# Optimization experiments

Measured on AMD Instinct MI355X. Metric: run time of the kernel, lower is better.

The kernel has to match this reference:

```python
import jax, jax.numpy as jnp
import numpy as np

TOP_K = 2  # n_heads / k in SigmaMoE


def setup_inputs() -> dict:
    key = jax.random.key(0)
    k1, k2, k3, k4 = jax.random.split(key, 4)
    B, S, d = 4, 2048, 512
    E, H = 32, 128  # n_experts, expert_size
    # init scales mirror reset_parameters (std ~ 1/sqrt(fan_in)) so sigmoid router is unsaturated
    x = jax.random.normal(k1, (B, S, d), dtype=jnp.float32)
    expert_sel = jax.random.normal(k2, (E, d), dtype=jnp.float32) / np.sqrt(d).astype(np.float32)
    keys = jax.random.normal(k3, (E, d, H), dtype=jnp.float32) / np.sqrt(d).astype(np.float32)
    values = jax.random.normal(k4, (E, H, d), dtype=jnp.float32) / np.sqrt(E * H).astype(np.float32)
    return {"x": x, "expert_sel": expert_sel, "keys": keys, "values": values}


def reference(x, expert_sel, keys, values):
    # x: [B, S, d]; expert_sel: [E, d]; keys: [E, d, H]; values: [E, H, v]
    B, S, d = x.shape
    E = keys.shape[0]
    xt = x.reshape(-1, d)                       # [T, d] tokens
    T = xt.shape[0]

    # Router: sigmoid gate + top-k expert selection (eval mode: no dropout, no sel_hist)
    sel = jax.nn.sigmoid(xt @ expert_sel.T)     # [T, E]
    sel_val, sel_idx = jax.lax.top_k(sel, TOP_K)  # [T, K] each; combine is order-invariant

    # Sparse routing weights as dense [T, E] mask (zero for unselected experts,
    # so unselected expert compute is exactly cancelled -> same math as cvmm dispatch/combine)
    w = jnp.zeros((T, E), dtype=xt.dtype).at[jnp.arange(T)[:, None], sel_idx].add(sel_val)

    # Expert FFN: scores = relu(x @ keys[e]); out = sum_e w[t,e] * scores @ values[e]
    h = jax.nn.relu(jnp.einsum('td,edh->teh', xt, keys))   # [T, E, H]
    out = jnp.einsum('teh,te,ehv->tv', h, w, values)       # [T, v]
    return out.reshape(B, S, -1)
```

## Files before the change

### kernel.cpp

```cpp
#include <hip/hip_runtime.h>

#define TT 8192
#define DD 512
#define EE 32
#define HH 128
#define NRB 256

typedef float f32x4 __attribute__((ext_vector_type(4)));
typedef __bf16 bf16x8 __attribute__((ext_vector_type(8)));
typedef unsigned short u16x8 __attribute__((ext_vector_type(8)));

__device__ __forceinline__ unsigned short f2bf(float f) {
  unsigned int u = __builtin_bit_cast(unsigned int, f);
  u = (u + 0x7FFFu + ((u >> 16) & 1u)) >> 16;
  return (unsigned short)u;
}
__device__ __forceinline__ float bf2f(unsigned short h) {
  return __builtin_bit_cast(float, (unsigned int)h << 16);
}

#define GLD16(g, l)                                                            \
  __builtin_amdgcn_global_load_lds(                                            \
      (const __attribute__((address_space(1))) unsigned int*)(g),              \
      (__attribute__((address_space(3))) unsigned int*)(l), 16, 0, 0)

__global__ __launch_bounds__(256) void prep_kernel(
    const float* __restrict__ x, const float* __restrict__ esel,
    const float* __restrict__ keys, const float* __restrict__ values,
    unsigned short* __restrict__ keysT, unsigned short* __restrict__ valuesT,
    unsigned short* __restrict__ xb, int* __restrict__ ccnt,
    int* __restrict__ etok, float* __restrict__ ew) {
  const int tid = threadIdx.x;
  int bid = blockIdx.x;
  if (bid < NRB) {
    __shared__ float ls[2][32][33];
    __shared__ int bcnt[EE], bcur[EE];
    const int tok0 = bid * 32;
    const int wv = tid >> 6, lane = tid & 63;
    const int mh = wv & 1;
    const int kh2 = wv >> 1;
    const int ll = lane & 15, lh = lane >> 4;
    const int row = tok0 + mh * 16 + ll;

    const float* xr = x + (size_t)row * DD + lh * 8;
    unsigned short* xbr = xb + (size_t)row * DD + lh * 8;
    const float* e0 = esel + (size_t)ll * DD + lh * 8;
    const float* e1 = esel + (size_t)(ll + 16) * DD + lh * 8;

    f32x4 acc0, acc1;
    acc0[0] = 0.f; acc0[1] = 0.f; acc0[2] = 0.f; acc0[3] = 0.f;
    acc1 = acc0;

#pragma unroll 2
    for (int kl = 0; kl < 8; kl++) {
      int k = kh2 * 8 + kl;
      float4 v0 = *(const float4*)(xr + k * 32);
      float4 v1 = *(const float4*)(xr + k * 32 + 4);
      float vv[8] = {v0.x, v0.y, v0.z, v0.w, v1.x, v1.y, v1.z, v1.w};
      bf16x8 ah, al, al2;
      unsigned short hs[8];
#pragma unroll
      for (int j = 0; j < 8; j++) {
        unsigned short hh = f2bf(vv[j]);
        float r1 = vv[j] - bf2f(hh);
        unsigned short lo = f2bf(r1);
        float r2 = r1 - bf2f(lo);
        hs[j] = hh;
        ah[j] = __builtin_bit_cast(__bf16, hh);
        al[j] = __builtin_bit_cast(__bf16, lo);
        al2[j] = __builtin_bit_cast(__bf16, f2bf(r2));
      }
      *(ushort4*)(xbr + k * 32) = *(ushort4*)&hs[0];
      *(ushort4*)(xbr + k * 32 + 4) = *(ushort4*)&hs[4];

      float4 c00 = *(const float4*)(e0 + k * 32);
      float4 c01 = *(const float4*)(e0 + k * 32 + 4);
      float4 c10 = *(const float4*)(e1 + k * 32);
      float4 c11 = *(const float4*)(e1 + k * 32 + 4);
      float ea[8] = {c00.x, c00.y, c00.z, c00.w, c01.x, c01.y, c01.z, c01.w};
      float eb[8] = {c10.x, c10.y, c10.z, c10.w, c11.x, c11.y, c11.z, c11.w};
      bf16x8 bh0, bl0, bm0, bh1, bl1, bm1;
#pragma unroll
      for (int j = 0; j < 8; j++) {
        unsigned short hh = f2bf(ea[j]);
        float r1 = ea[j] - bf2f(hh);
        unsigned short lo = f2bf(r1);
        float r2 = r1 - bf2f(lo);
        bh0[j] = __builtin_bit_cast(__bf16, hh);
        bl0[j] = __builtin_bit_cast(__bf16, lo);
        bm0[j] = __builtin_bit_cast(__bf16, f2bf(r2));
        hh = f2bf(eb[j]);
        r1 = eb[j] - bf2f(hh);
        lo = f2bf(r1);
        r2 = r1 - bf2f(lo);
        bh1[j] = __builtin_bit_cast(__bf16, hh);
        bl1[j] = __builtin_bit_cast(__bf16, lo);
        bm1[j] = __builtin_bit_cast(__bf16, f2bf(r2));
      }

      acc0 = __builtin_amdgcn_mfma_f32_16x16x32_bf16(ah, bh0, acc0, 0, 0, 0);
      acc0 = __builtin_amdgcn_mfma_f32_16x16x32_bf16(ah, bl0, acc0, 0, 0, 0);
      acc0 = __builtin_amdgcn_mfma_f32_16x16x32_bf16(al, bh0, acc0, 0, 0, 0);
      acc0 = __builtin_amdgcn_mfma_f32_16x16x32_bf16(ah, bm0, acc0, 0, 0, 0);
      acc0 = __builtin_amdgcn_mfma_f32_16x16x32_bf16(al, bl0, acc0, 0, 0, 0);
      acc0 = __builtin_amdgcn_mfma_f32_16x16x32_bf16(al2, bh0, acc0, 0, 0, 0);

      acc1 = __builtin_amdgcn_mfma_f32_16x16x32_bf16(ah, bh1, acc1, 0, 0, 0);
      acc1 = __builtin_amdgcn_mfma_f32_16x16x32_bf16(ah, bl1, acc1, 0, 0, 0);
      acc1 = __builtin_amdgcn_mfma_f32_16x16x32_bf16(al, bh1, acc1, 0, 0, 0);
      acc1 = __builtin_amdgcn_mfma_f32_16x16x32_bf16(ah, bm1, acc1, 0, 0, 0);
      acc1 = __builtin_amdgcn_mfma_f32_16x16x32_bf16(al, bl1, acc1, 0, 0, 0);
      acc1 = __builtin_amdgcn_mfma_f32_16x16x32_bf16(al2, bh1, acc1, 0, 0, 0);
    }

#pragma unroll
    for (int r = 0; r < 4; r++) {
      ls[kh2][mh * 16 + lh * 4 + r][ll] = acc0[r];
      ls[kh2][mh * 16 + lh * 4 + r][16 + ll] = acc1[r];
    }
    if (tid < EE) bcnt[tid] = 0;
    __syncthreads();

    int i0 = 0, i1 = 0;
    float w0 = 0.f, w1 = 0.f;
    if (tid < 32) {
      float m0 = -3.4e38f;
#pragma unroll
      for (int e2 = 0; e2 < EE; e2++) {
        float v = ls[0][tid][e2] + ls[1][tid][e2];
        if (v > m0) { m0 = v; i0 = e2; }
      }
      float m1 = -3.4e38f;
      i1 = (i0 == 0) ? 1 : 0;
#pragma unroll
      for (int e2 = 0; e2 < EE; e2++) {
        float v = ls[0][tid][e2] + ls[1][tid][e2];
        if (e2 != i0 && v > m1) { m1 = v; i1 = e2; }
      }
      w0 = 1.f / (1.f + expf(-m0));
      w1 = 1.f / (1.f + expf(-m1));
      atomicAdd(&bcnt[i0], 1);
      atomicAdd(&bcnt[i1], 1);
    }
    __syncthreads();
    if (tid < EE) { ccnt[tid * NRB + bid] = bcnt[tid]; bcur[tid] = 0; }
    __syncthreads();
    if (tid < 32) {
      int t = tok0 + tid;
      int p0 = atomicAdd(&bcur[i0], 1);
      etok[((size_t)i0 * NRB + bid) * 32 + p0] = t;
      ew[((size_t)i0 * NRB + bid) * 32 + p0] = w0;
      int p1 = atomicAdd(&bcur[i1], 1);
      etok[((size_t)i1 * NRB + bid) * 32 + p1] = t | (1 << 20);
      ew[((size_t)i1 * NRB + bid) * 32 + p1] = w1;
    }
    return;
  }
  bid -= NRB;
  __shared__ float tile[64][68];
  const float* src;
  unsigned short* dst;
  int R, C, r0, c0, e;
  if (bid < 512) {
    e = bid >> 4; int sub = bid & 15;
    R = DD; C = HH; r0 = (sub >> 1) * 64; c0 = (sub & 1) * 64;
    src = keys; dst = keysT;
  } else {
    bid -= 512;
    e = bid >> 4; int sub = bid & 15;
    R = HH; C = DD; r0 = (sub & 1) * 64; c0 = (sub >> 1) * 64;
    src = values; dst = valuesT;
  }
  const int rl = tid >> 2, cq = (tid & 3) * 16;
  const float* s0 = src + ((size_t)e * R + r0 + rl) * C + c0 + cq;
#pragma unroll
  for (int i = 0; i < 4; i++) *(float4*)&tile[rl][cq + 4 * i] = *(const float4*)(s0 + 4 * i);
  __syncthreads();
  unsigned short* d0 = dst + ((size_t)e * C + c0 + rl) * R + r0 + cq;
#pragma unroll
  for (int i = 0; i < 4; i++) {
    ushort4 v;
    v.x = f2bf(tile[cq + 4 * i + 0][rl]);
    v.y = f2bf(tile[cq + 4 * i + 1][rl]);
    v.z = f2bf(tile[cq + 4 * i + 2][rl]);
    v.w = f2bf(tile[cq + 4 * i + 3][rl]);
    *(ushort4*)(d0 + 4 * i) = v;
  }
}

__global__ __launch_bounds__(512) void moe_gemm_kernel(
    const unsigned short* __restrict__ xb,
    const unsigned short* __restrict__ keysT,
    const unsigned short* __restrict__ valuesT,
    const int* __restrict__ ccnt,
    const int* __restrict__ etok,
    const float* __restrict__ ew,
    unsigned short* __restrict__ yb) {
  const int e = blockIdx.x;
  const int base = blockIdx.y * 64;

  __shared__ int csc[NRB];
  __shared__ unsigned short stage_buf[2][8192];
  __shared__ unsigned short h_swz[8192];
  __shared__ int tok_s[64];
  __shared__ int srow_s[64];
  __shared__ float w_s[64];

  const int tid = threadIdx.x;

  if (tid < NRB) csc[tid] = ccnt[e * NRB + tid];
  __syncthreads();
  for (int off = 1; off < NRB; off <<= 1) {
    int v = 0;
    if (tid < NRB) { v = csc[tid]; if (tid >= off) v += csc[tid - off]; }
    __syncthreads();
    if (tid < NRB) csc[tid] = v;
    __syncthreads();
  }
  const int cnt = csc[NRB - 1];
  if (base >= cnt) return;

  const int lane = tid & 63;
  const int wv = tid >> 6;
  const int wm = wv & 3;
  const int wn = wv >> 2;
  const int ll = lane & 15, lh = lane >> 4;

  const unsigned short* kT = keysT + (size_t)e * HH * DD;
  const unsigned short* vT = valuesT + (size_t)e * DD * HH;

  auto stage_b1 = [&](int c, int b) {
#pragma unroll
    for (int i = 0; i < 2; i++) {
      int P = (i * 512 + tid) * 16;
      int n = P >> 7;
      int q = P & 127;
      const char* g = (const char*)(kT + (size_t)n * DD + c * 64) + (q ^ ((n & 7) << 4));
      char* l = (char*)stage_buf[b] + (i * 512 + (tid & ~63)) * 16;
      GLD16(g, l);
    }
  };
  auto stage_b2 = [&](int c, int b) {
#pragma unroll
    for (int i = 0; i < 2; i++) {
      int P = (i * 512 + tid) * 16;
      int r = P >> 8;
      int q = P & 255;
      const char* g = (const char*)(vT + (size_t)(c * 64 + r) * HH) + (q ^ ((r & 7) << 4));
      char* l = (char*)stage_buf[b] + (i * 512 + (tid & ~63)) * 16;
      GLD16(g, l);
    }
  };

  stage_b1(0, 0);
  if (tid < 64) {
    int i = base + tid;
    bool valid = i < cnt;
    int ie = valid ? i : (cnt - 1);
    int lo = 0, hi = NRB - 1;
    while (lo < hi) { int mid = (lo + hi) >> 1; if (csc[mid] > ie) hi = mid; else lo = mid + 1; }
    int prev = lo ? csc[lo - 1] : 0;
    size_t cell = ((size_t)e * NRB + lo) * 32 + (ie - prev);
    int v = etok[cell];
    int t = v & 0xFFFFF;
    tok_s[tid] = t;
    srow_s[tid] = valid ? ((v >> 20) * (TT + 1) + t) : TT;
    w_s[tid] = valid ? ew[cell] : 0.f;
  }
  __syncthreads();

  const unsigned short* ap = xb + (size_t)tok_s[wm * 16 + ll] * DD;

  f32x4 acc[4];
#pragma unroll
  for (int n = 0; n < 4; n++) { acc[n][0] = 0.f; acc[n][1] = 0.f; acc[n][2] = 0.f; acc[n][3] = 0.f; }

  for (int c = 0; c < 8; c++) {
    if (c < 7) stage_b1(c + 1, (c + 1) & 1);
    else       stage_b2(0, 0);
    const char* sb = (const char*)stage_buf[c & 1];
#pragma unroll
    for (int kkl = 0; kkl < 2; kkl++) {
      bf16x8 af = *(const bf16x8*)(ap + c * 64 + kkl * 32 + lh * 8);
#pragma unroll
      for (int nt = 0; nt < 4; nt++) {
        int n = wn * 64 + nt * 16 + ll;
        int boff = n * 128 + ((kkl * 64 + lh * 16) ^ ((n & 7) << 4));
        bf16x8 bfr = *(const bf16x8*)(sb + boff);
        acc[nt] = __builtin_amdgcn_mfma_f32_16x16x32_bf16(af, bfr, acc[nt], 0, 0, 0);
      }
    }
    __syncthreads();
  }

#pragma unroll
  for (int nt = 0; nt < 4; nt++) {
#pragma unroll
    for (int r = 0; r < 4; r++) {
      int row = wm * 16 + lh * 4 + r;
      int col = wn * 64 + nt * 16 + ll;
      int off = row * 256 + ((col * 2) ^ ((row & 7) << 4));
      *(unsigned short*)((char*)h_swz + off) = f2bf(fmaxf(acc[nt][r], 0.f));
    }
  }
  __syncthreads();

  bf16x8 a2[4];
#pragma unroll
  for (int kk = 0; kk < 4; kk++) {
    int row = wm * 16 + ll;
    int off = row * 256 + ((kk * 64 + lh * 16) ^ ((row & 7) << 4));
    a2[kk] = *(const bf16x8*)((const char*)h_swz + off);
  }

  float wr[4];
#pragma unroll
  for (int r = 0; r < 4; r++) wr[r] = w_s[wm * 16 + lh * 4 + r];

  __syncthreads();
  unsigned short* y_lds = h_swz;

  for (int c = 0; c < 8; c++) {
    if (c < 7) stage_b2(c + 1, (c + 1) & 1);
    const char* sb = (const char*)stage_buf[c & 1];
#pragma unroll
    for (int ntl = 0; ntl < 2; ntl++) {
      f32x4 c2;
      c2[0] = 0.f; c2[1] = 0.f; c2[2] = 0.f; c2[3] = 0.f;
#pragma unroll
      for (int kk = 0; kk < 4; kk++) {
        int r = wn * 32 + ntl * 16 + ll;
        int boff = r * 256 + ((kk * 64 + lh * 16) ^ ((r & 7) << 4));
        bf16x8 bfr = *(const bf16x8*)(sb + boff);
        c2 = __builtin_amdgcn_mfma_f32_16x16x32_bf16(a2[kk], bfr, c2, 0, 0, 0);
      }
      int colb = wn * 32 + ntl * 16 + ll;
#pragma unroll
      for (int r = 0; r < 4; r++) {
        int row = wm * 16 + lh * 4 + r;
        int off = row * 128 + ((colb * 2) ^ ((row & 7) << 4));
        *(unsigned short*)((char*)y_lds + off) = f2bf(c2[r] * wr[r]);
      }
    }
    __syncthreads();
    {
      int rr = tid >> 3, g = tid & 7;
      int off = rr * 128 + ((g * 16) ^ ((rr & 7) << 4));
      u16x8 v = *(const u16x8*)((const char*)y_lds + off);
      *(u16x8*)(yb + (size_t)srow_s[rr] * DD + c * 64 + g * 8) = v;
    }
    __syncthreads();
  }
}

__global__ __launch_bounds__(256) void combine_kernel(const unsigned short* __restrict__ yb,
                                                      float* __restrict__ out) {
  size_t i = ((size_t)blockIdx.x * 256 + threadIdx.x) * 8;
  u16x8 a = *(const u16x8*)(yb + i);
  u16x8 b = *(const u16x8*)(yb + (size_t)(TT + 1) * DD + i);
  float4 o0, o1;
  o0.x = bf2f(a[0]) + bf2f(b[0]);
  o0.y = bf2f(a[1]) + bf2f(b[1]);
  o0.z = bf2f(a[2]) + bf2f(b[2]);
  o0.w = bf2f(a[3]) + bf2f(b[3]);
  o1.x = bf2f(a[4]) + bf2f(b[4]);
  o1.y = bf2f(a[5]) + bf2f(b[5]);
  o1.z = bf2f(a[6]) + bf2f(b[6]);
  o1.w = bf2f(a[7]) + bf2f(b[7]);
  *(float4*)(out + i) = o0;
  *(float4*)(out + i + 4) = o1;
}

extern "C" void kernel_launch(void* const* d_in, const int* in_sizes, int n_in,
                              void* d_out, int out_size, void* d_ws, size_t ws_size,
                              hipStream_t stream) {
  const float* x = (const float*)d_in[0];
  const float* esel = (const float*)d_in[1];
  const float* keys = (const float*)d_in[2];
  const float* values = (const float*)d_in[3];
  float* out = (float*)d_out;

  char* p = (char*)d_ws;
  unsigned short* xb = (unsigned short*)p;      p += (size_t)TT * DD * 2;
  unsigned short* keysT = (unsigned short*)p;   p += (size_t)EE * DD * HH * 2;
  unsigned short* valuesT = (unsigned short*)p; p += (size_t)EE * DD * HH * 2;
  int* ccnt = (int*)p;                          p += (size_t)EE * NRB * 4;
  int* etok = (int*)p;                          p += (size_t)EE * NRB * 32 * 4;
  float* ew = (float*)p;                        p += (size_t)EE * NRB * 32 * 4;
  unsigned short* yb = (unsigned short*)p;      p += (size_t)2 * (TT + 1) * DD * 2;

  prep_kernel<<<NRB + 1024, 256, 0, stream>>>(x, esel, keys, values, keysT, valuesT,
                                              xb, ccnt, etok, ew);
  moe_gemm_kernel<<<dim3(EE, TT / 64), 512, 0, stream>>>(xb, keysT, valuesT, ccnt, etok, ew, yb);
  combine_kernel<<<(TT * DD / 8) / 256, 256, 0, stream>>>(yb, out);
}
```

Before: 51.22 us.

## Precompute per-expert scans and compact work list to replace oversized GEMM grid

```diff
diff --git a/kernel.cpp b/kernel.cpp
--- a/kernel.cpp
+++ b/kernel.cpp
@@ -29,9 +29,10 @@
     const float* __restrict__ keys, const float* __restrict__ values,
     unsigned short* __restrict__ keysT, unsigned short* __restrict__ valuesT,
     unsigned short* __restrict__ xb, int* __restrict__ ccnt,
-    int* __restrict__ etok, float* __restrict__ ew) {
+    int* __restrict__ etok, float* __restrict__ ew, int* __restrict__ wl_cnt) {
   const int tid = threadIdx.x;
   int bid = blockIdx.x;
+  if (bid == 0 && tid == 0) *wl_cnt = 0;
   if (bid < NRB) {
     __shared__ float ls[2][32][33];
     __shared__ int bcnt[EE], bcur[EE];
@@ -188,18 +189,56 @@
   }
 }
 
+__global__ __launch_bounds__(NRB) void scan_kernel(
+    const int* __restrict__ ccnt, const int* __restrict__ etok,
+    const float* __restrict__ ew, int* __restrict__ cntg,
+    int* __restrict__ etok2, float* __restrict__ ew2,
+    int* __restrict__ wl, int* __restrict__ wl_cnt) {
+  __shared__ int csc[NRB];
+  __shared__ int sbase;
+  const int e = blockIdx.x, tid = threadIdx.x;
+  csc[tid] = ccnt[e * NRB + tid];
+  __syncthreads();
+  for (int off = 1; off < NRB; off <<= 1) {
+    int v = csc[tid];
+    if (tid >= off) v += csc[tid - off];
+    __syncthreads();
+    csc[tid] = v;
+    __syncthreads();
+  }
+  const int cnt = csc[NRB - 1];
+  const int s = tid ? csc[tid - 1] : 0;
+  const int c = csc[tid] - s;
+  const int* st = etok + ((size_t)e * NRB + tid) * 32;
+  const float* sw = ew + ((size_t)e * NRB + tid) * 32;
+  for (int j = 0; j < c; j++) {
+    etok2[(size_t)e * TT + s + j] = st[j];
+    ew2[(size_t)e * TT + s + j] = sw[j];
+  }
+  if (tid == 0) {
+    cntg[e] = cnt;
+    sbase = atomicAdd(wl_cnt, (cnt + 63) >> 6);
+  }
+  __syncthreads();
+  if (tid < ((cnt + 63) >> 6)) wl[sbase + tid] = (e << 16) | tid;
+}
+
 __global__ __launch_bounds__(512) void moe_gemm_kernel(
     const unsigned short* __restrict__ xb,
     const unsigned short* __restrict__ keysT,
     const unsigned short* __restrict__ valuesT,
-    const int* __restrict__ ccnt,
-    const int* __restrict__ etok,
-    const float* __restrict__ ew,
+    const int* __restrict__ cntg,
+    const int* __restrict__ etok2,
+    const float* __restrict__ ew2,
+    const int* __restrict__ wl, const int* __restrict__ wl_cnt,
     unsigned short* __restrict__ yb) {
-  const int e = blockIdx.x;
-  const int base = blockIdx.y * 64;
-
-  __shared__ int csc[NRB];
+  const int bid = blockIdx.x;
+  if (bid >= *wl_cnt) return;
+  const int wle = wl[bid];
+  const int e = wle >> 16;
+  const int base = (wle & 0xFFFF) * 64;
+  const int cnt = cntg[e];
+
   __shared__ unsigned short stage_buf[2][8192];
   __shared__ unsigned short h_swz[8192];
   __shared__ int tok_s[64];
@@ -207,19 +246,6 @@
   __shared__ float w_s[64];
 
   const int tid = threadIdx.x;
-
-  if (tid < NRB) csc[tid] = ccnt[e * NRB + tid];
-  __syncthreads();
-  for (int off = 1; off < NRB; off <<= 1) {
-    int v = 0;
-    if (tid < NRB) { v = csc[tid]; if (tid >= off) v += csc[tid - off]; }
-    __syncthreads();
-    if (tid < NRB) csc[tid] = v;
-    __syncthreads();
-  }
-  const int cnt = csc[NRB - 1];
-  if (base >= cnt) return;
-
   const int lane = tid & 63;
   const int wv = tid >> 6;
   const int wm = wv & 3;
@@ -257,15 +283,11 @@
     int i = base + tid;
     bool valid = i < cnt;
     int ie = valid ? i : (cnt - 1);
-    int lo = 0, hi = NRB - 1;
-    while (lo < hi) { int mid = (lo + hi) >> 1; if (csc[mid] > ie) hi = mid; else lo = mid + 1; }
-    int prev = lo ? csc[lo - 1] : 0;
-    size_t cell = ((size_t)e * NRB + lo) * 32 + (ie - prev);
-    int v = etok[cell];
+    int v = etok2[(size_t)e * TT + ie];
     int t = v & 0xFFFFF;
     tok_s[tid] = t;
     srow_s[tid] = valid ? ((v >> 20) * (TT + 1) + t) : TT;
-    w_s[tid] = valid ? ew[cell] : 0.f;
+    w_s[tid] = valid ? ew2[(size_t)e * TT + ie] : 0.f;
   }
   __syncthreads();
 
@@ -387,10 +409,16 @@
   int* ccnt = (int*)p;                          p += (size_t)EE * NRB * 4;
   int* etok = (int*)p;                          p += (size_t)EE * NRB * 32 * 4;
   float* ew = (float*)p;                        p += (size_t)EE * NRB * 32 * 4;
+  int* cntg = (int*)p;                          p += 256;
+  int* etok2 = (int*)p;                         p += (size_t)EE * TT * 4;
+  float* ew2 = (float*)p;                       p += (size_t)EE * TT * 4;
+  int* wl = (int*)p;                            p += 512 * 4;
+  int* wl_cnt = (int*)p;                        p += 256;
   unsigned short* yb = (unsigned short*)p;      p += (size_t)2 * (TT + 1) * DD * 2;
 
   prep_kernel<<<NRB + 1024, 256, 0, stream>>>(x, esel, keys, values, keysT, valuesT,
-                                              xb, ccnt, etok, ew);
-  moe_gemm_kernel<<<dim3(EE, TT / 64), 512, 0, stream>>>(xb, keysT, valuesT, ccnt, etok, ew, yb);
+                                              xb, ccnt, etok, ew, wl_cnt);
+  scan_kernel<<<EE, NRB, 0, stream>>>(ccnt, etok, ew, cntg, etok2, ew2, wl, wl_cnt);
+  moe_gemm_kernel<<<512, 512, 0, stream>>>(xb, keysT, valuesT, cntg, etok2, ew2, wl, wl_cnt, yb);
   combine_kernel<<<(TT * DD / 8) / 256, 256, 0, stream>>>(yb, out);
 }
```

Measured after the change: 54.83 us. 1.07x slower.

## Widen prep kernel to 512 threads and use wave-shuffle prefix scan in GEMM

Applied to the files above, without the earlier changes.

```diff
diff --git a/kernel.cpp b/kernel.cpp
--- a/kernel.cpp
+++ b/kernel.cpp
@@ -24,7 +24,7 @@
       (const __attribute__((address_space(1))) unsigned int*)(g),              \
       (__attribute__((address_space(3))) unsigned int*)(l), 16, 0, 0)
 
-__global__ __launch_bounds__(256) void prep_kernel(
+__global__ __launch_bounds__(512) void prep_kernel(
     const float* __restrict__ x, const float* __restrict__ esel,
     const float* __restrict__ keys, const float* __restrict__ values,
     unsigned short* __restrict__ keysT, unsigned short* __restrict__ valuesT,
@@ -33,12 +33,12 @@
   const int tid = threadIdx.x;
   int bid = blockIdx.x;
   if (bid < NRB) {
-    __shared__ float ls[2][32][33];
+    __shared__ float ls[4][32][33];
     __shared__ int bcnt[EE], bcur[EE];
     const int tok0 = bid * 32;
     const int wv = tid >> 6, lane = tid & 63;
     const int mh = wv & 1;
-    const int kh2 = wv >> 1;
+    const int kq = wv >> 1;
     const int ll = lane & 15, lh = lane >> 4;
     const int row = tok0 + mh * 16 + ll;
 
@@ -52,8 +52,8 @@
     acc1 = acc0;
 
 #pragma unroll 2
-    for (int kl = 0; kl < 8; kl++) {
-      int k = kh2 * 8 + kl;
+    for (int kl = 0; kl < 4; kl++) {
+      int k = kq * 4 + kl;
       float4 v0 = *(const float4*)(xr + k * 32);
       float4 v1 = *(const float4*)(xr + k * 32 + 4);
       float vv[8] = {v0.x, v0.y, v0.z, v0.w, v1.x, v1.y, v1.z, v1.w};
@@ -115,8 +115,8 @@
 
 #pragma unroll
     for (int r = 0; r < 4; r++) {
-      ls[kh2][mh * 16 + lh * 4 + r][ll] = acc0[r];
-      ls[kh2][mh * 16 + lh * 4 + r][16 + ll] = acc1[r];
+      ls[kq][mh * 16 + lh * 4 + r][ll] = acc0[r];
+      ls[kq][mh * 16 + lh * 4 + r][16 + ll] = acc1[r];
     }
     if (tid < EE) bcnt[tid] = 0;
     __syncthreads();
@@ -127,14 +127,14 @@
       float m0 = -3.4e38f;
 #pragma unroll
       for (int e2 = 0; e2 < EE; e2++) {
-        float v = ls[0][tid][e2] + ls[1][tid][e2];
+        float v = ls[0][tid][e2] + ls[1][tid][e2] + ls[2][tid][e2] + ls[3][tid][e2];
         if (v > m0) { m0 = v; i0 = e2; }
       }
       float m1 = -3.4e38f;
       i1 = (i0 == 0) ? 1 : 0;
 #pragma unroll
       for (int e2 = 0; e2 < EE; e2++) {
-        float v = ls[0][tid][e2] + ls[1][tid][e2];
+        float v = ls[0][tid][e2] + ls[1][tid][e2] + ls[2][tid][e2] + ls[3][tid][e2];
         if (e2 != i0 && v > m1) { m1 = v; i1 = e2; }
       }
       w0 = 1.f / (1.f + expf(-m0));
@@ -171,14 +171,14 @@
     R = HH; C = DD; r0 = (sub & 1) * 64; c0 = (sub >> 1) * 64;
     src = values; dst = valuesT;
   }
-  const int rl = tid >> 2, cq = (tid & 3) * 16;
+  const int rl = tid >> 3, cq = (tid & 7) * 8;
   const float* s0 = src + ((size_t)e * R + r0 + rl) * C + c0 + cq;
-#pragma unroll
-  for (int i = 0; i < 4; i++) *(float4*)&tile[rl][cq + 4 * i] = *(const float4*)(s0 + 4 * i);
+  *(float4*)&tile[rl][cq] = *(const float4*)(s0);
+  *(float4*)&tile[rl][cq + 4] = *(const float4*)(s0 + 4);
   __syncthreads();
   unsigned short* d0 = dst + ((size_t)e * C + c0 + rl) * R + r0 + cq;
 #pragma unroll
-  for (int i = 0; i < 4; i++) {
+  for (int i = 0; i < 2; i++) {
     ushort4 v;
     v.x = f2bf(tile[cq + 4 * i + 0][rl]);
     v.y = f2bf(tile[cq + 4 * i + 1][rl]);
@@ -200,6 +200,7 @@
   const int base = blockIdx.y * 64;
 
   __shared__ int csc[NRB];
+  __shared__ int cnt_s;
   __shared__ unsigned short stage_buf[2][8192];
   __shared__ unsigned short h_swz[8192];
   __shared__ int tok_s[64];
@@ -207,21 +208,28 @@
   __shared__ float w_s[64];
 
   const int tid = threadIdx.x;
-
-  if (tid < NRB) csc[tid] = ccnt[e * NRB + tid];
-  __syncthreads();
-  for (int off = 1; off < NRB; off <<= 1) {
-    int v = 0;
-    if (tid < NRB) { v = csc[tid]; if (tid >= off) v += csc[tid - off]; }
-    __syncthreads();
-    if (tid < NRB) csc[tid] = v;
-    __syncthreads();
-  }
-  const int cnt = csc[NRB - 1];
-  if (base >= cnt) return;
-
   const int lane = tid & 63;
   const int wv = tid >> 6;
+
+  if (wv == 0) {
+    int4 c4 = *(const int4*)(ccnt + e * NRB + lane * 4);
+    int s0 = c4.x, s1 = s0 + c4.y, s2 = s1 + c4.z, s3 = s2 + c4.w;
+    int tot = s3;
+    for (int off = 1; off < 64; off <<= 1) {
+      int n = __shfl_up(tot, off);
+      if (lane >= off) tot += n;
+    }
+    int b0 = tot - s3;
+    csc[lane * 4 + 0] = b0 + s0;
+    csc[lane * 4 + 1] = b0 + s1;
+    csc[lane * 4 + 2] = b0 + s2;
+    csc[lane * 4 + 3] = b0 + s3;
+    if (lane == 63) cnt_s = tot;
+  }
+  __syncthreads();
+  const int cnt = cnt_s;
+  if (base >= cnt) return;
+
   const int wm = wv & 3;
   const int wn = wv >> 2;
   const int ll = lane & 15, lh = lane >> 4;
@@ -389,7 +397,7 @@
   float* ew = (float*)p;                        p += (size_t)EE * NRB * 32 * 4;
   unsigned short* yb = (unsigned short*)p;      p += (size_t)2 * (TT + 1) * DD * 2;
 
-  prep_kernel<<<NRB + 1024, 256, 0, stream>>>(x, esel, keys, values, keysT, valuesT,
+  prep_kernel<<<NRB + 1024, 512, 0, stream>>>(x, esel, keys, values, keysT, valuesT,
                                               xb, ccnt, etok, ew);
   moe_gemm_kernel<<<dim3(EE, TT / 64), 512, 0, stream>>>(xb, keysT, valuesT, ccnt, etok, ew, yb);
   combine_kernel<<<(TT * DD / 8) / 256, 256, 0, stream>>>(yb, out);
```

Result: faster. 48.23 us, median of 2 (-5.8%).
